# Performance work log

Hardware: AMD Instinct MI355X
Metric: run time of the kernel (lower is better)

## Reference

```python
import jax, jax.numpy as jnp
import numpy as np

B, L, H, N = 8, 2048, 512, 64  # batch, seq_len, d_model, SSM state size


def setup_inputs() -> dict:
    key = jax.random.key(0)
    ks = jax.random.split(key, 10)
    x = jax.random.normal(ks[0], (B, L, H), jnp.float32)
    # S4D-style parameters (diagonal SSM, S4D-Lin init)
    log_dt = jnp.log(1e-3) + jax.random.uniform(ks[1], (H,), jnp.float32) * (jnp.log(1e-1) - jnp.log(1e-3))
    A_re = -0.5 * jnp.ones((H, N), jnp.float32)
    A_im = jnp.tile(np.pi * jnp.arange(N, dtype=np.float32), (H, 1))
    C_re = jax.random.normal(ks[2], (H, N), jnp.float32) * (0.5 ** 0.5)
    C_im = jax.random.normal(ks[3], (H, N), jnp.float32) * (0.5 ** 0.5)
    D_skip = jax.random.normal(ks[4], (H,), jnp.float32)
    # S4 output linear (GLU): d_model -> 2*d_model, then gated
    W_out = jax.random.normal(ks[5], (2 * H, H), jnp.float32) / np.sqrt(H)
    b_out = jnp.zeros((2 * H,), jnp.float32)
    # LayerNorms
    g1 = jnp.ones((H,), jnp.float32); beta1 = jnp.zeros((H,), jnp.float32)
    g2 = jnp.ones((H,), jnp.float32); beta2 = jnp.zeros((H,), jnp.float32)
    # 1x1 conv FFN (kernel_size=1 => pointwise linear), d_ff = d_model
    W1 = jax.random.normal(ks[6], (H, H), jnp.float32) / np.sqrt(H)
    bc1 = jnp.zeros((H,), jnp.float32)
    W2 = jax.random.normal(ks[7], (H, H), jnp.float32) / np.sqrt(H)
    bc2 = jnp.zeros((H,), jnp.float32)
    return dict(x=x, log_dt=log_dt, A_re=A_re, A_im=A_im, C_re=C_re, C_im=C_im,
                D_skip=D_skip, W_out=W_out, b_out=b_out, g1=g1, beta1=beta1,
                g2=g2, beta2=beta2, W1=W1, bc1=bc1, W2=W2, bc2=bc2)


def _layer_norm(x, g, b):
    mu = jnp.mean(x, axis=-1, keepdims=True)
    var = jnp.mean((x - mu) ** 2, axis=-1, keepdims=True)
    return (x - mu) / jnp.sqrt(var + 1e-5) * g + b


def _s4(x, log_dt, A_re, A_im, C_re, C_im, D_skip, W_out, b_out):
    # x: (B, L, H) channels-last (transposed=False)
    Lx = x.shape[1]
    dt = jnp.exp(log_dt)                       # (H,)
    A = A_re + 1j * A_im                       # (H, N) diagonal state matrix
    dtA = A * dt[:, None]
    # ZOH discretization of C: Ct = C * (exp(dt*A) - 1) / A
    Ct = (C_re + 1j * C_im) * ((jnp.exp(dtA) - 1.0) / A)
    # Vandermonde kernel: K[h, l] = 2 Re sum_n Ct[h,n] exp(dt*A[h,n]*l)
    l = jnp.arange(Lx, dtype=jnp.float32)
    K = 2.0 * jnp.real(jnp.einsum('hn,hnl->hl', Ct, jnp.exp(dtA[:, :, None] * l)))
    # FFT long convolution (linear conv via zero-padded circular conv)
    u = jnp.swapaxes(x, 1, 2)                  # (B, H, L)
    n = 2 * Lx
    y = jnp.fft.irfft(jnp.fft.rfft(u, n) * jnp.fft.rfft(K, n)[None], n)[..., :Lx]
    y = y + D_skip[None, :, None] * u          # skip connection D*u
    y = jax.nn.gelu(y)                         # S4 default activation
    # output linear + GLU (S4 default postact)
    z = jnp.einsum('bhl,fh->bfl', y, W_out) + b_out[None, :, None]
    a, g = jnp.split(z, 2, axis=1)
    y = a * jax.nn.sigmoid(g)
    return jnp.swapaxes(y, 1, 2)               # (B, L, H)


def reference(x, log_dt, A_re, A_im, C_re, C_im, D_skip, W_out, b_out,
              g1, beta1, g2, beta2, W1, bc1, W2, bc2):
    new_x = _s4(x, log_dt, A_re, A_im, C_re, C_im, D_skip, W_out, b_out)
    x = x + new_x
    x = _layer_norm(x, g1, beta1)
    # FFN via 1x1 convs (pointwise linears); dropout is identity in eval
    y = jax.nn.relu(jnp.einsum('blh,fh->blf', x, W1) + bc1)
    y = jnp.einsum('blf,hf->blh', y, W2) + bc2
    return _layer_norm(x + y, g2, beta2)
```

## Files before the change

kernel.cpp:

```cpp
#include <hip/hip_runtime.h>
#include <cstddef>
#include <cstdint>

#define B_DIM 8
#define L_DIM 2048
#define H_DIM 512
#define N_DIM 64
#define HN (H_DIM * N_DIM)
#define BLH (B_DIM * L_DIM * H_DIM)
#define M_DIM (B_DIM * L_DIM)

typedef unsigned short u16;
typedef short bf16x8 __attribute__((ext_vector_type(8)));
typedef float floatx4 __attribute__((ext_vector_type(4)));

__device__ __forceinline__ float sigmoidf_(float v) {
    return 1.0f / (1.0f + __expf(-v));
}

__device__ __forceinline__ float gelu_tanh_(float x) {
    float x3 = x * x * x;
    float z = 0.7978845608028654f * fmaf(0.044715f, x3, x);
    float e = __expf(-2.0f * fabsf(z));
    float th = (1.0f - e) / (1.0f + e);
    th = copysignf(th, z);
    return 0.5f * x * (1.0f + th);
}

__device__ __forceinline__ u16 f2b(float f) {
    unsigned u = __float_as_uint(f);
    unsigned r = (u + 0x7fffu + ((u >> 16) & 1u)) >> 16;
    return (u16)r;
}
__device__ __forceinline__ float b2f(u16 u) {
    return __uint_as_float(((unsigned)u) << 16);
}
__device__ __forceinline__ void unpack2(unsigned u, float& a, float& b) {
    a = __uint_as_float(u << 16);
    b = __uint_as_float(u & 0xffff0000u);
}
__device__ __forceinline__ unsigned pack2(float a, float b) {
    return (unsigned)f2b(a) | ((unsigned)f2b(b) << 16);
}

__device__ __forceinline__ void csq(float& r, float& i) {
    float nr = r * r - i * i;
    i = 2.0f * r * i;
    r = nr;
}

__global__ __launch_bounds__(256) void cast_kernel(
    const float* __restrict__ src, u16* __restrict__ dst)
{
    int i = blockIdx.x * 256 + threadIdx.x;
    float4 v = *(const float4*)(src + (size_t)i * 4);
    uint2 p;
    p.x = pack2(v.x, v.y);
    p.y = pack2(v.z, v.w);
    *(uint2*)(dst + (size_t)i * 4) = p;
}

__global__ __launch_bounds__(256) void precompute_kernel(
    const float* __restrict__ log_dt, const float* __restrict__ A_re,
    const float* __restrict__ A_im, const float* __restrict__ C_re,
    const float* __restrict__ C_im, float* __restrict__ P)
{
    int i = blockIdx.x * 256 + threadIdx.x;
    if (i >= HN) return;
    int h = i >> 6;
    float dt = expf(log_dt[h]);
    float Ar = A_re[i], Ai = A_im[i];
    float ar = dt * Ar, ai = dt * Ai;
    float e = expf(ar);
    float wr = e * cosf(ai);
    float wi = e * sinf(ai);
    float em1r = wr - 1.0f, em1i = wi;
    float inv = 1.0f / fmaf(Ar, Ar, Ai * Ai);
    float qr = fmaf(em1r, Ar, em1i * Ai) * inv;
    float qi = fmaf(em1i, Ar, -(em1r * Ai)) * inv;
    float Cr = C_re[i], Ci = C_im[i];
    float ctr = Cr * qr - Ci * qi;
    float cti = Cr * qi + Ci * qr;
    P[i]          = wr;
    P[HN + i]     = wi;
    P[2 * HN + i] = 2.0f * ctr;
    P[3 * HN + i] = 2.0f * cti;
}

__global__ __launch_bounds__(256) void ktab_kernel(
    const float* __restrict__ P, float* __restrict__ Ktab)
{
    int wv = threadIdx.x >> 6, lane = threadIdx.x & 63;
    int h = blockIdx.x * 4 + wv;
    int pidx = (h << 6) + lane;
    float wr = P[pidx], wi = P[HN + pidx];
    float c2r = P[2 * HN + pidx], c2i = P[3 * HN + pidx];
    float pr = 1.0f, pi = 0.0f;
    for (int tau = 0; tau < 64; ++tau) {
        float term = c2r * pr - c2i * pi;
        #pragma unroll
        for (int m = 32; m > 0; m >>= 1) term += __shfl_xor(term, m, 64);
        if (lane == 0) Ktab[(h << 6) + tau] = term;
        float nr = pr * wr - pi * wi, ni = pr * wi + pi * wr;
        pr = nr; pi = ni;
    }
}

__global__ __launch_bounds__(256) void toepfill_kernel(
    const float* __restrict__ Ktab, u16* __restrict__ Toep_bf)
{
    int idx = blockIdx.x * 256 + threadIdx.x;
    int h = idx >> 12;
    int rem = idx & 4095;
    int tt = rem >> 6, j = rem & 63;
    u16 v = 0;
    if (j <= tt) v = f2b(Ktab[(h << 6) + (tt - j)]);
    Toep_bf[idx] = v;
}

__global__ __launch_bounds__(256) void xtrans_kernel(
    const float* __restrict__ x, u16* __restrict__ XT)
{
    __shared__ float tile[32][33];
    int b  = blockIdx.z;
    int l0 = blockIdx.x * 32;
    int h0 = blockIdx.y * 32;
    int tx = threadIdx.x & 31;
    int ty = threadIdx.x >> 5;
    #pragma unroll
    for (int r = 0; r < 4; ++r)
        tile[ty + r * 8][tx] = x[((size_t)b * L_DIM + l0 + ty + r * 8) * H_DIM + h0 + tx];
    __syncthreads();
    #pragma unroll
    for (int r = 0; r < 4; ++r)
        XT[((size_t)b * H_DIM + h0 + ty + r * 8) * L_DIM + l0 + tx] = f2b(tile[tx][ty + r * 8]);
}

__global__ __launch_bounds__(256) void ssm_chunk_kernel(
    const u16* __restrict__ XT, const float* __restrict__ P,
    const u16* __restrict__ Toep_bf, const float* __restrict__ D_skip,
    u16* __restrict__ YT)
{
    __shared__ u16 U[128 * 72];
    __shared__ u16 S[128 * 136];
    __shared__ u16 EVT[13312];
    u16* E  = EVT;
    u16* Tp = EVT;
    u16* V  = EVT + 4608;

    const int h    = blockIdx.x;
    const int b0   = blockIdx.y * 4;
    const int t    = threadIdx.x;
    const int lane = t & 63;
    const int wv   = t >> 6;
    const int lm   = lane & 15, lq = lane >> 4;

    const int pidx = (h << 6) + lane;
    const float wr  = P[pidx],          wi  = P[HN + pidx];
    const float c2r = P[2 * HN + pidx], c2i = P[3 * HN + pidx];

    #pragma unroll
    for (int r = 0; r < 4; ++r) {
        int idx = t + r * 256;
        int row = idx >> 3, ch = idx & 7;
        const u16* gp = XT + (((size_t)(b0 + (row >> 5)) * H_DIM + h) << 11)
                           + ((row & 31) << 6) + (ch << 3);
        *(uint4*)&U[row * 72 + ch * 8] = *(const uint4*)gp;
    }

    float bwr, bwi;
    {
        float g16r = wr, g16i = wi;
        csq(g16r, g16i); csq(g16r, g16i); csq(g16r, g16i); csq(g16r, g16i);
        if (wv == 0)      { bwr = 1.0f; bwi = 0.0f; }
        else if (wv == 1) { bwr = g16r; bwi = g16i; }
        else if (wv == 2) { bwr = g16r; bwi = g16i; csq(bwr, bwi); }
        else {
            float g32r = g16r, g32i = g16i; csq(g32r, g32i);
            bwr = g32r * g16r - g32i * g16i;
            bwi = g32r * g16i + g32i * g16r;
        }
    }

    {
        float pr = bwr, pi = bwi;
        #pragma unroll
        for (int jk = 0; jk < 16; ++jk) {
            int k = (wv << 4) + jk;
            int j = 63 - k;
            E[(2 * lane) * 72 + j]     = f2b(pr);
            E[(2 * lane + 1) * 72 + j] = f2b(pi);
            float nr = pr * wr - pi * wi, ni = pr * wi + pi * wr;
            pr = nr; pi = ni;
        }
    }
    __syncthreads();

    {
        const int wm = wv >> 1, wn = wv & 1;
        floatx4 acc[4][4] = {};
        #pragma unroll
        for (int ks = 0; ks < 2; ++ks) {
            bf16x8 af[4], bfv[4];
            #pragma unroll
            for (int i = 0; i < 4; ++i)
                af[i] = *(const bf16x8*)&E[(wm * 64 + i * 16 + lm) * 72 + ks * 32 + lq * 8];
            #pragma unroll
            for (int j = 0; j < 4; ++j)
                bfv[j] = *(const bf16x8*)&U[(wn * 64 + j * 16 + lm) * 72 + ks * 32 + lq * 8];
            #pragma unroll
            for (int i = 0; i < 4; ++i) {
                #pragma unroll
                for (int j = 0; j < 4; ++j)
                    acc[i][j] = __builtin_amdgcn_mfma_f32_16x16x32_bf16(af[i], bfv[j], acc[i][j], 0, 0, 0);
            }
        }
        #pragma unroll
        for (int i = 0; i < 4; ++i) {
            #pragma unroll
            for (int j = 0; j < 4; ++j) {
                int ncol = wn * 64 + j * 16 + lm;
                int m0   = wm * 64 + i * 16 + lq * 4;
                u16 pk[4];
                #pragma unroll
                for (int r = 0; r < 4; ++r) pk[r] = f2b(acc[i][j][r]);
                *(uint2*)&S[ncol * 136 + m0] = *(uint2*)pk;
            }
        }
    }
    __syncthreads();

    {
        float pr = bwr, pi = bwi;
        {
            float nr = pr * wr - pi * wi, ni = pr * wi + pi * wr;
            pr = nr; pi = ni;
        }
        #pragma unroll
        for (int jk = 1; jk <= 16; ++jk) {
            int tr = (wv << 4) + jk - 1;
            float qr = c2r * pr - c2i * pi;
            float qi = c2r * pi + c2i * pr;
            V[tr * 136 + 2 * lane]     = f2b(qr);
            V[tr * 136 + 2 * lane + 1] = f2b(-qi);
            float nr = pr * wr - pi * wi, ni = pr * wi + pi * wr;
            pr = nr; pi = ni;
        }
        #pragma unroll
        for (int r = 0; r < 2; ++r) {
            int idx = t + r * 256;
            int row = idx >> 3, ch = idx & 7;
            *(uint4*)&Tp[row * 72 + ch * 8] =
                *(const uint4*)&Toep_bf[((size_t)h << 12) + (row << 6) + (ch << 3)];
        }
        float wTr = wr, wTi = wi;
        csq(wTr, wTi); csq(wTr, wTi); csq(wTr, wTi);
        csq(wTr, wTi); csq(wTr, wTi); csq(wTr, wTi);
        float Sr = 0.0f, Si = 0.0f;
        const int n2 = lane * 2;
        for (int c = 0; c < 32; ++c) {
            int base = (wv * 32 + c) * 136 + n2;
            unsigned lv = *(unsigned*)&S[base];
            float lr, li;
            unpack2(lv, lr, li);
            *(unsigned*)&S[base] = pack2(Sr, Si);
            float nSr = wTr * Sr - wTi * Si + lr;
            Si = wTr * Si + wTi * Sr + li;
            Sr = nSr;
        }
    }
    __syncthreads();

    {
        const float Dh = D_skip[h];
        floatx4 acc[4][2] = {};
        #pragma unroll
        for (int ks = 0; ks < 6; ++ks) {
            bf16x8 af[4], bfv[2];
            if (ks < 2) {
                #pragma unroll
                for (int i = 0; i < 4; ++i)
                    af[i] = *(const bf16x8*)&Tp[(i * 16 + lm) * 72 + ks * 32 + lq * 8];
                #pragma unroll
                for (int j = 0; j < 2; ++j)
                    bfv[j] = *(const bf16x8*)&U[(wv * 32 + j * 16 + lm) * 72 + ks * 32 + lq * 8];
            } else {
                #pragma unroll
                for (int i = 0; i < 4; ++i)
                    af[i] = *(const bf16x8*)&V[(i * 16 + lm) * 136 + (ks - 2) * 32 + lq * 8];
                #pragma unroll
                for (int j = 0; j < 2; ++j)
                    bfv[j] = *(const bf16x8*)&S[(wv * 32 + j * 16 + lm) * 136 + (ks - 2) * 32 + lq * 8];
            }
            #pragma unroll
            for (int i = 0; i < 4; ++i) {
                #pragma unroll
                for (int j = 0; j < 2; ++j)
                    acc[i][j] = __builtin_amdgcn_mfma_f32_16x16x32_bf16(af[i], bfv[j], acc[i][j], 0, 0, 0);
            }
        }
        #pragma unroll
        for (int j = 0; j < 2; ++j) {
            int ncol = wv * 32 + j * 16 + lm;
            int bloc = ncol >> 5, c = ncol & 31;
            size_t gbase = (((size_t)(b0 + bloc) * H_DIM + h) << 11) + (c << 6);
            #pragma unroll
            for (int i = 0; i < 4; ++i) {
                int t0 = i * 16 + lq * 4;
                u16 upk[4];
                *(uint2*)upk = *(const uint2*)&U[ncol * 72 + t0];
                u16 opk[4];
                #pragma unroll
                for (int r = 0; r < 4; ++r) {
                    float uvv = b2f(upk[r]);
                    float yv = gelu_tanh_(fmaf(Dh, uvv, acc[i][j][r]));
                    opk[r] = f2b(yv);
                }
                *(uint2*)&YT[gbase + t0] = *(uint2*)opk;
            }
        }
    }
}

__global__ __launch_bounds__(256) void ytrans_kernel(
    const u16* __restrict__ YT, u16* __restrict__ Y)
{
    __shared__ u16 tile[32][33];
    int b  = blockIdx.z;
    int l0 = blockIdx.x * 32;
    int h0 = blockIdx.y * 32;
    int tx = threadIdx.x & 31;
    int ty = threadIdx.x >> 5;
    #pragma unroll
    for (int r = 0; r < 4; ++r)
        tile[ty + r * 8][tx] = YT[((size_t)b * H_DIM + h0 + ty + r * 8) * L_DIM + l0 + tx];
    __syncthreads();
    #pragma unroll
    for (int r = 0; r < 4; ++r)
        Y[((size_t)b * L_DIM + l0 + ty + r * 8) * H_DIM + h0 + tx] = tile[tx][ty + r * 8];
}

__device__ __forceinline__ void stage_tile_128x32(
    const u16* __restrict__ g, u16* lds, int row0, int k0)
{
    const int t = threadIdx.x;
    #pragma unroll
    for (int r = 0; r < 2; ++r) {
        int row = (t >> 2) + r * 64;
        int col = (t & 3) * 8;
        const u16* gp = g + (size_t)(row0 + row) * 512 + k0 + col;
        __builtin_amdgcn_global_load_lds(
            (const __attribute__((address_space(1))) unsigned int*)gp,
            (__attribute__((address_space(3))) unsigned int*)(lds + (size_t)t * 8 + (size_t)r * 2048),
            16, 0, 0);
    }
}

__global__ __launch_bounds__(256) void gemm1_glu_kernel(
    const u16* __restrict__ A, const u16* __restrict__ Wo,
    const float* __restrict__ bo, const float* __restrict__ x,
    u16* __restrict__ out)
{
    __shared__ u16 As[128 * 32];
    __shared__ u16 Ba[128 * 32];
    __shared__ u16 Bg[128 * 32];
    const int t    = threadIdx.x;
    const int lane = t & 63;
    const int wv   = t >> 6;
    const int wm   = wv >> 1, wn = wv & 1;
    const int lm   = lane & 15, lq = lane >> 4;
    const int m0   = blockIdx.x * 128, n0 = blockIdx.y * 128;
    floatx4 accA[4][4] = {};
    floatx4 accG[4][4] = {};
    for (int k0 = 0; k0 < 512; k0 += 32) {
        stage_tile_128x32(A, As, m0, k0);
        stage_tile_128x32(Wo, Ba, n0, k0);
        stage_tile_128x32(Wo, Bg, 512 + n0, k0);
        __syncthreads();
        bf16x8 af[4], ba[4], bg[4];
        #pragma unroll
        for (int i = 0; i < 4; ++i)
            af[i] = *(const bf16x8*)&As[(wm * 64 + i * 16 + lm) * 32 + lq * 8];
        #pragma unroll
        for (int j = 0; j < 4; ++j) {
            ba[j] = *(const bf16x8*)&Ba[(wn * 64 + j * 16 + lm) * 32 + lq * 8];
            bg[j] = *(const bf16x8*)&Bg[(wn * 64 + j * 16 + lm) * 32 + lq * 8];
        }
        #pragma unroll
        for (int i = 0; i < 4; ++i) {
            #pragma unroll
            for (int j = 0; j < 4; ++j) {
                accA[i][j] = __builtin_amdgcn_mfma_f32_16x16x32_bf16(af[i], ba[j], accA[i][j], 0, 0, 0);
                accG[i][j] = __builtin_amdgcn_mfma_f32_16x16x32_bf16(af[i], bg[j], accG[i][j], 0, 0, 0);
            }
        }
        __syncthreads();
    }
    #pragma unroll
    for (int j = 0; j < 4; ++j) {
        int n = n0 + wn * 64 + j * 16 + lm;
        float bav = bo[n], bgv = bo[512 + n];
        #pragma unroll
        for (int i = 0; i < 4; ++i) {
            #pragma unroll
            for (int r = 0; r < 4; ++r) {
                int m = m0 + wm * 64 + i * 16 + lq * 4 + r;
                float av = accA[i][j][r] + bav;
                float gv = accG[i][j][r] + bgv;
                float xv = x[(size_t)m * 512 + n];
                out[(size_t)m * 512 + n] = f2b(fmaf(av, sigmoidf_(gv), xv));
            }
        }
    }
}

template<int EPI>
__global__ __launch_bounds__(256) void gemm_bt_bf_kernel(
    const u16* __restrict__ A, const u16* __restrict__ Bw,
    const float* __restrict__ bias, u16* __restrict__ C)
{
    __shared__ u16 As[128 * 32];
    __shared__ u16 Bs[128 * 32];
    const int t    = threadIdx.x;
    const int lane = t & 63;
    const int wv   = t >> 6;
    const int wm   = wv >> 1, wn = wv & 1;
    const int lm   = lane & 15, lq = lane >> 4;
    const int m0   = blockIdx.x * 128, n0 = blockIdx.y * 128;
    floatx4 acc[4][4] = {};
    for (int k0 = 0; k0 < 512; k0 += 32) {
        stage_tile_128x32(A, As, m0, k0);
        stage_tile_128x32(Bw, Bs, n0, k0);
        __syncthreads();
        bf16x8 af[4], bfr[4];
        #pragma unroll
        for (int i = 0; i < 4; ++i)
            af[i] = *(const bf16x8*)&As[(wm * 64 + i * 16 + lm) * 32 + lq * 8];
        #pragma unroll
        for (int j = 0; j < 4; ++j)
            bfr[j] = *(const bf16x8*)&Bs[(wn * 64 + j * 16 + lm) * 32 + lq * 8];
        #pragma unroll
        for (int i = 0; i < 4; ++i) {
            #pragma unroll
            for (int j = 0; j < 4; ++j)
                acc[i][j] = __builtin_amdgcn_mfma_f32_16x16x32_bf16(af[i], bfr[j], acc[i][j], 0, 0, 0);
        }
        __syncthreads();
    }
    #pragma unroll
    for (int j = 0; j < 4; ++j) {
        int n = n0 + wn * 64 + j * 16 + lm;
        float bv = bias[n];
        #pragma unroll
        for (int i = 0; i < 4; ++i) {
            #pragma unroll
            for (int r = 0; r < 4; ++r) {
                int m = m0 + wm * 64 + i * 16 + lq * 4 + r;
                float v = acc[i][j][r] + bv;
                if (EPI == 1) v = fmaxf(v, 0.0f);
                C[(size_t)m * 512 + n] = f2b(v);
            }
        }
    }
}

template<bool HASRES, bool F32OUT>
__global__ __launch_bounds__(256) void ln_bf_kernel(
    const u16* __restrict__ in, const u16* __restrict__ res,
    const float* __restrict__ gamma, const float* __restrict__ beta,
    u16* __restrict__ outb, float* __restrict__ outf)
{
    int w    = threadIdx.x >> 6;
    int lane = threadIdx.x & 63;
    size_t row  = (size_t)blockIdx.x * 4 + w;
    size_t base = row * 512 + lane * 8;
    uint4 raw = *(const uint4*)(in + base);
    float v[8];
    unpack2(raw.x, v[0], v[1]); unpack2(raw.y, v[2], v[3]);
    unpack2(raw.z, v[4], v[5]); unpack2(raw.w, v[6], v[7]);
    if (HASRES) {
        uint4 rr = *(const uint4*)(res + base);
        float rv[8];
        unpack2(rr.x, rv[0], rv[1]); unpack2(rr.y, rv[2], rv[3]);
        unpack2(rr.z, rv[4], rv[5]); unpack2(rr.w, rv[6], rv[7]);
        #pragma unroll
        for (int i = 0; i < 8; ++i) v[i] += rv[i];
    }
    float s = 0.0f, sq = 0.0f;
    #pragma unroll
    for (int i = 0; i < 8; ++i) { s += v[i]; sq = fmaf(v[i], v[i], sq); }
    #pragma unroll
    for (int m = 32; m > 0; m >>= 1) {
        s  += __shfl_xor(s, m, 64);
        sq += __shfl_xor(sq, m, 64);
    }
    float mu  = s * (1.0f / 512.0f);
    float var = sq * (1.0f / 512.0f) - mu * mu;
    float rs  = rsqrtf(var + 1e-5f);
    float g[8], bt[8];
    *(float4*)&g[0]  = *(const float4*)(gamma + lane * 8);
    *(float4*)&g[4]  = *(const float4*)(gamma + lane * 8 + 4);
    *(float4*)&bt[0] = *(const float4*)(beta + lane * 8);
    *(float4*)&bt[4] = *(const float4*)(beta + lane * 8 + 4);
    float o[8];
    #pragma unroll
    for (int i = 0; i < 8; ++i)
        o[i] = fmaf((v[i] - mu) * rs, g[i], bt[i]);
    if (F32OUT) {
        *(float4*)(outf + base)     = *(float4*)&o[0];
        *(float4*)(outf + base + 4) = *(float4*)&o[4];
    } else {
        uint4 p;
        p.x = pack2(o[0], o[1]); p.y = pack2(o[2], o[3]);
        p.z = pack2(o[4], o[5]); p.w = pack2(o[6], o[7]);
        *(uint4*)(outb + base) = p;
    }
}

extern "C" void kernel_launch(void* const* d_in, const int* in_sizes, int n_in,
                              void* d_out, int out_size, void* d_ws, size_t ws_size,
                              hipStream_t stream)
{
    (void)in_sizes; (void)n_in; (void)out_size; (void)ws_size;
    const float* x      = (const float*)d_in[0];
    const float* log_dt = (const float*)d_in[1];
    const float* A_re   = (const float*)d_in[2];
    const float* A_im   = (const float*)d_in[3];
    const float* C_re   = (const float*)d_in[4];
    const float* C_im   = (const float*)d_in[5];
    const float* D_skip = (const float*)d_in[6];
    const float* W_out  = (const float*)d_in[7];
    const float* b_out  = (const float*)d_in[8];
    const float* g1     = (const float*)d_in[9];
    const float* beta1  = (const float*)d_in[10];
    const float* g2     = (const float*)d_in[11];
    const float* beta2  = (const float*)d_in[12];
    const float* W1     = (const float*)d_in[13];
    const float* bc1    = (const float*)d_in[14];
    const float* W2     = (const float*)d_in[15];
    const float* bc2    = (const float*)d_in[16];
    float* out = (float*)d_out;

    char*  wsb    = (char*)d_ws;
    float* P      = (float*)wsb;
    float* Ktab   = (float*)(wsb + 4 * HN * 4);
    u16*   Toep   = (u16*)(wsb + 4 * HN * 4 + 512 * 64 * 4);
    u16*   Wobf   = Toep + 512 * 4096;
    u16*   W1bf   = Wobf + 1024 * 512;
    u16*   W2bf   = W1bf + 512 * 512;
    u16*   r1     = W2bf + 512 * 512;
    u16*   r2     = r1 + BLH;
    u16*   r3     = r2 + BLH;

    cast_kernel<<<512, 256, 0, stream>>>(W_out, Wobf);
    cast_kernel<<<256, 256, 0, stream>>>(W1, W1bf);
    cast_kernel<<<256, 256, 0, stream>>>(W2, W2bf);
    precompute_kernel<<<HN / 256, 256, 0, stream>>>(log_dt, A_re, A_im, C_re, C_im, P);
    ktab_kernel<<<128, 256, 0, stream>>>(P, Ktab);
    toepfill_kernel<<<8192, 256, 0, stream>>>(Ktab, Toep);
    xtrans_kernel<<<dim3(L_DIM / 32, H_DIM / 32, B_DIM), 256, 0, stream>>>(x, r1);
    ssm_chunk_kernel<<<dim3(H_DIM, 2), 256, 0, stream>>>(r1, P, Toep, D_skip, r2);
    ytrans_kernel<<<dim3(L_DIM / 32, H_DIM / 32, B_DIM), 256, 0, stream>>>(r2, r3);
    gemm1_glu_kernel<<<dim3(M_DIM / 128, 4), 256, 0, stream>>>(r3, Wobf, b_out, x, r2);
    ln_bf_kernel<false, false><<<M_DIM / 4, 256, 0, stream>>>(r2, nullptr, g1, beta1, r1, nullptr);
    gemm_bt_bf_kernel<1><<<dim3(M_DIM / 128, 4), 256, 0, stream>>>(r1, W1bf, bc1, r3);
    gemm_bt_bf_kernel<0><<<dim3(M_DIM / 128, 4), 256, 0, stream>>>(r3, W2bf, bc2, r2);
    ln_bf_kernel<true, true><<<M_DIM / 4, 256, 0, stream>>>(r2, r1, g2, beta2, nullptr, out);
}
```

Baseline: 267.8 us.

## Double-buffer LDS tiles in GEMM kernels to overlap loads with MFMA

Both GEMM kernels (GLU output projection and FFN linears) now keep two LDS buffers per operand. Each iteration issues async global-to-LDS loads for the next K tile before running MFMAs on the current one, with one barrier per iteration instead of two. This is meant to hide global memory latency behind compute, at the cost of doubled shared memory, which may lower occupancy. Correctness depends on the manual vmcnt wait and barrier ordering.

```diff
diff --git a/kernel.cpp b/kernel.cpp
--- a/kernel.cpp
+++ b/kernel.cpp
@@ -361,9 +361,9 @@
     const float* __restrict__ bo, const float* __restrict__ x,
     u16* __restrict__ out)
 {
-    __shared__ u16 As[128 * 32];
-    __shared__ u16 Ba[128 * 32];
-    __shared__ u16 Bg[128 * 32];
+    __shared__ u16 As[2][128 * 32];
+    __shared__ u16 Ba[2][128 * 32];
+    __shared__ u16 Bg[2][128 * 32];
     const int t    = threadIdx.x;
     const int lane = t & 63;
     const int wv   = t >> 6;
@@ -372,19 +372,31 @@
     const int m0   = blockIdx.x * 128, n0 = blockIdx.y * 128;
     floatx4 accA[4][4] = {};
     floatx4 accG[4][4] = {};
+
+    stage_tile_128x32(A, As[0], m0, 0);
+    stage_tile_128x32(Wo, Ba[0], n0, 0);
+    stage_tile_128x32(Wo, Bg[0], 512 + n0, 0);
+    asm volatile("s_waitcnt vmcnt(0)" ::: "memory");
+    __builtin_amdgcn_s_barrier();
+    asm volatile("" ::: "memory");
+
+    int cur = 0;
     for (int k0 = 0; k0 < 512; k0 += 32) {
-        stage_tile_128x32(A, As, m0, k0);
-        stage_tile_128x32(Wo, Ba, n0, k0);
-        stage_tile_128x32(Wo, Bg, 512 + n0, k0);
-        __syncthreads();
+        const int nx = cur ^ 1;
+        const bool more = (k0 + 32 < 512);
+        if (more) {
+            stage_tile_128x32(A, As[nx], m0, k0 + 32);
+            stage_tile_128x32(Wo, Ba[nx], n0, k0 + 32);
+            stage_tile_128x32(Wo, Bg[nx], 512 + n0, k0 + 32);
+        }
         bf16x8 af[4], ba[4], bg[4];
         #pragma unroll
         for (int i = 0; i < 4; ++i)
-            af[i] = *(const bf16x8*)&As[(wm * 64 + i * 16 + lm) * 32 + lq * 8];
+            af[i] = *(const bf16x8*)&As[cur][(wm * 64 + i * 16 + lm) * 32 + lq * 8];
         #pragma unroll
         for (int j = 0; j < 4; ++j) {
-            ba[j] = *(const bf16x8*)&Ba[(wn * 64 + j * 16 + lm) * 32 + lq * 8];
-            bg[j] = *(const bf16x8*)&Bg[(wn * 64 + j * 16 + lm) * 32 + lq * 8];
+            ba[j] = *(const bf16x8*)&Ba[cur][(wn * 64 + j * 16 + lm) * 32 + lq * 8];
+            bg[j] = *(const bf16x8*)&Bg[cur][(wn * 64 + j * 16 + lm) * 32 + lq * 8];
         }
         #pragma unroll
         for (int i = 0; i < 4; ++i) {
@@ -394,7 +406,13 @@
                 accG[i][j] = __builtin_amdgcn_mfma_f32_16x16x32_bf16(af[i], bg[j], accG[i][j], 0, 0, 0);
             }
         }
-        __syncthreads();
+        if (more) {
+            asm volatile("" ::: "memory");
+            asm volatile("s_waitcnt vmcnt(0)" ::: "memory");
+            __builtin_amdgcn_s_barrier();
+            asm volatile("" ::: "memory");
+        }
+        cur = nx;
     }
     #pragma unroll
     for (int j = 0; j < 4; ++j) {
@@ -419,8 +437,8 @@
     const u16* __restrict__ A, const u16* __restrict__ Bw,
     const float* __restrict__ bias, u16* __restrict__ C)
 {
-    __shared__ u16 As[128 * 32];
-    __shared__ u16 Bs[128 * 32];
+    __shared__ u16 As[2][128 * 32];
+    __shared__ u16 Bs[2][128 * 32];
     const int t    = threadIdx.x;
     const int lane = t & 63;
     const int wv   = t >> 6;
@@ -428,24 +446,41 @@
     const int lm   = lane & 15, lq = lane >> 4;
     const int m0   = blockIdx.x * 128, n0 = blockIdx.y * 128;
     floatx4 acc[4][4] = {};
+
+    stage_tile_128x32(A, As[0], m0, 0);
+    stage_tile_128x32(Bw, Bs[0], n0, 0);
+    asm volatile("s_waitcnt vmcnt(0)" ::: "memory");
+    __builtin_amdgcn_s_barrier();
+    asm volatile("" ::: "memory");
+
+    int cur = 0;
     for (int k0 = 0; k0 < 512; k0 += 32) {
-        stage_tile_128x32(A, As, m0, k0);
-        stage_tile_128x32(Bw, Bs, n0, k0);
-        __syncthreads();
+        const int nx = cur ^ 1;
+        const bool more = (k0 + 32 < 512);
+        if (more) {
+            stage_tile_128x32(A, As[nx], m0, k0 + 32);
+            stage_tile_128x32(Bw, Bs[nx], n0, k0 + 32);
+        }
         bf16x8 af[4], bfr[4];
         #pragma unroll
         for (int i = 0; i < 4; ++i)
-            af[i] = *(const bf16x8*)&As[(wm * 64 + i * 16 + lm) * 32 + lq * 8];
+            af[i] = *(const bf16x8*)&As[cur][(wm * 64 + i * 16 + lm) * 32 + lq * 8];
         #pragma unroll
         for (int j = 0; j < 4; ++j)
-            bfr[j] = *(const bf16x8*)&Bs[(wn * 64 + j * 16 + lm) * 32 + lq * 8];
+            bfr[j] = *(const bf16x8*)&Bs[cur][(wn * 64 + j * 16 + lm) * 32 + lq * 8];
         #pragma unroll
         for (int i = 0; i < 4; ++i) {
             #pragma unroll
             for (int j = 0; j < 4; ++j)
                 acc[i][j] = __builtin_amdgcn_mfma_f32_16x16x32_bf16(af[i], bfr[j], acc[i][j], 0, 0, 0);
         }
-        __syncthreads();
+        if (more) {
+            asm volatile("" ::: "memory");
+            asm volatile("s_waitcnt vmcnt(0)" ::: "memory");
+            __builtin_amdgcn_s_barrier();
+            asm volatile("" ::: "memory");
+        }
+        cur = nx;
     }
     #pragma unroll
     for (int j = 0; j < 4; ++j) {
```

After: 281.6 us. +5.1%, slower.
